# Performance work log

Hardware: AMD Instinct MI355X
Metric: run time of the kernel (lower is better)

The kernel has to match this reference:

```python
import jax, jax.numpy as jnp
import numpy as np

B, S, D, H = 8, 1024, 768, 12
DH = D // H


def setup_inputs() -> dict:
    key = jax.random.key(0)
    ks = jax.random.split(key, 6)
    scale = 1.0 / np.sqrt(D)
    return {
        "inputs": jax.random.normal(ks[0], (B, S, D), dtype=jnp.float32),
        "Wq": jax.random.normal(ks[1], (D, D), dtype=jnp.float32) * scale,
        "bq": jnp.zeros((D,), jnp.float32),
        "Wk": jax.random.normal(ks[2], (D, D), dtype=jnp.float32) * scale,
        "bk": jnp.zeros((D,), jnp.float32),
        "Wv": jax.random.normal(ks[3], (D, D), dtype=jnp.float32) * scale,
        "bv": jnp.zeros((D,), jnp.float32),
        "Wo": jax.random.normal(ks[4], (D, D), dtype=jnp.float32) * scale,
        "bo": jnp.zeros((D,), jnp.float32),
    }


def _split_heads(x):
    # [B,S,D] -> [B,H,S,DH]
    b, s, _ = x.shape
    return x.reshape(b, s, H, DH).transpose(0, 2, 1, 3)


def reference(inputs, Wq, bq, Wk, bk, Wv, bv, Wo, bo):
    q = _split_heads(inputs @ Wq + bq)
    k = _split_heads(inputs @ Wk + bk)
    v = _split_heads(inputs @ Wv + bv)
    # scaled dot-product attention; scale = sqrt(projection_dim)
    scores = jnp.einsum("bhqd,bhkd->bhqk", q, k) / jnp.sqrt(jnp.float32(DH))
    weights = jax.nn.softmax(scores, axis=-1)
    attn = jnp.einsum("bhqk,bhkd->bhqd", weights, v)
    attn = attn.transpose(0, 2, 1, 3).reshape(inputs.shape[0], -1, D)
    return attn @ Wo + bo
```

## Files before the change

kernel.cpp:

```cpp
#include <hip/hip_runtime.h>
#include <math.h>

#define B 8
#define S 1024
#define D 768
#define H 12
#define DH 64
#define M_TOT (B * S)

typedef short bf16x8 __attribute__((ext_vector_type(8)));
typedef float f32x4 __attribute__((ext_vector_type(4)));

__device__ __forceinline__ unsigned short f2bf(float x) {
    unsigned u = __builtin_bit_cast(unsigned, x);
    u = (u + 0x7FFFu + ((u >> 16) & 1u)) >> 16;
    return (unsigned short)u;
}
__device__ __forceinline__ unsigned pk2bf(float a, float b) {
    return (unsigned)f2bf(a) | ((unsigned)f2bf(b) << 16);
}

__device__ __forceinline__ void async16(const unsigned short* g, unsigned short* l) {
    __builtin_amdgcn_global_load_lds((const __attribute__((address_space(1))) void*)g,
                                     (__attribute__((address_space(3))) void*)l, 16, 0, 0);
}

__global__ __launch_bounds__(256) void conv_bf16(const float* __restrict__ src,
                                                 unsigned short* __restrict__ dst) {
    const int i = (blockIdx.x * 256 + threadIdx.x) * 4;
    const float4 v = *(const float4*)&src[i];
    ushort4 o;
    o.x = f2bf(v.x); o.y = f2bf(v.y); o.z = f2bf(v.z); o.w = f2bf(v.w);
    *(ushort4*)&dst[i] = o;
}

__global__ __launch_bounds__(256) void wtrans(const float* W0, const float* W1,
                                              const float* W2, const float* W3,
                                              unsigned short* T0, unsigned short* T1,
                                              unsigned short* T2, unsigned short* T3) {
    const float* Wsrc[4] = {W0, W1, W2, W3};
    unsigned short* Tdst[4] = {T0, T1, T2, T3};
    const float* Wm = Wsrc[blockIdx.z];
    unsigned short* Tm = Tdst[blockIdx.z];
    __shared__ float tile[64][65];
    const int t = threadIdx.x;
    const int r = t >> 4, c4 = (t & 15) * 4;
    const int k0 = blockIdx.x * 64, n0 = blockIdx.y * 64;
#pragma unroll
    for (int rr = 0; rr < 4; ++rr) {
        const float4 v = *(const float4*)&Wm[(size_t)(k0 + r + rr * 16) * D + n0 + c4];
        tile[r + rr * 16][c4 + 0] = v.x;
        tile[r + rr * 16][c4 + 1] = v.y;
        tile[r + rr * 16][c4 + 2] = v.z;
        tile[r + rr * 16][c4 + 3] = v.w;
    }
    __syncthreads();
#pragma unroll
    for (int rr = 0; rr < 4; ++rr) {
        const int nr = r + rr * 16;
        ushort4 o;
        o.x = f2bf(tile[c4 + 0][nr]);
        o.y = f2bf(tile[c4 + 1][nr]);
        o.z = f2bf(tile[c4 + 2][nr]);
        o.w = f2bf(tile[c4 + 3][nr]);
        *(ushort4*)&Tm[(size_t)(n0 + nr) * D + k0 + c4] = o;
    }
}

__global__ __launch_bounds__(256) void gemm_qkv(const unsigned short* __restrict__ A,
                                                const unsigned short* __restrict__ Wtq,
                                                const unsigned short* __restrict__ Wtk,
                                                const unsigned short* __restrict__ Wtv,
                                                const float* __restrict__ bq,
                                                const float* __restrict__ bk,
                                                const float* __restrict__ bv,
                                                unsigned short* __restrict__ Qb,
                                                unsigned short* __restrict__ Kb,
                                                unsigned short* __restrict__ Vtb) {
    __shared__ unsigned short At[128 * 32];
    __shared__ unsigned short Bs[128 * 32];
    const int z = blockIdx.z;
    const unsigned short* Bt = (z == 0) ? Wtq : (z == 1) ? Wtk : Wtv;
    const float* bias = (z == 0) ? bq : (z == 1) ? bk : bv;
    const float scale = (z == 0) ? 0.125f : 1.0f;

    const int t = threadIdx.x;
    const int w = t >> 6, lane = t & 63;
    const int quad = lane >> 4, l15 = lane & 15;
    const int m0 = blockIdx.x * 128, n0 = blockIdx.y * 128;
    const int wm = (w & 1) * 64, wn = (w >> 1) * 64;
    const int srow = lane >> 2, scol = (lane & 3) * 8;

    f32x4 acc[4][4];
#pragma unroll
    for (int i = 0; i < 4; ++i)
#pragma unroll
        for (int j = 0; j < 4; ++j) acc[i][j] = (f32x4){0.f, 0.f, 0.f, 0.f};

    for (int kt = 0; kt < D / 32; ++kt) {
        const int k0 = kt * 32;
        __syncthreads();
#pragma unroll
        for (int c = 0; c < 2; ++c) {
            const int cc = w * 2 + c;
            const int row = cc * 16 + srow;
            async16(&A[(size_t)(m0 + row) * D + k0 + scol], &At[cc * 512]);
            async16(&Bt[(size_t)(n0 + row) * D + k0 + scol], &Bs[cc * 512]);
        }
        __syncthreads();
        bf16x8 af[4], bfr[4];
#pragma unroll
        for (int i = 0; i < 4; ++i)
            af[i] = *(const bf16x8*)&At[(wm + i * 16 + l15) * 32 + quad * 8];
#pragma unroll
        for (int j = 0; j < 4; ++j)
            bfr[j] = *(const bf16x8*)&Bs[(wn + j * 16 + l15) * 32 + quad * 8];
#pragma unroll
        for (int i = 0; i < 4; ++i)
#pragma unroll
            for (int j = 0; j < 4; ++j)
                acc[i][j] = __builtin_amdgcn_mfma_f32_16x16x32_bf16(af[i], bfr[j], acc[i][j], 0, 0, 0);
    }

#pragma unroll
    for (int j = 0; j < 4; ++j) {
        const int col = n0 + wn + j * 16 + l15;
        const float bv2 = bias[col];
#pragma unroll
        for (int i = 0; i < 4; ++i) {
            const int row0 = m0 + wm + i * 16 + quad * 4;
            if (z < 2) {
                unsigned short* C = (z == 0) ? Qb : Kb;
#pragma unroll
                for (int r = 0; r < 4; ++r)
                    C[(size_t)(row0 + r) * D + col] = f2bf((acc[i][j][r] + bv2) * scale);
            } else {
                const int h = col >> 6, dh = col & 63;
                const int bb = row0 >> 10, s0 = row0 & 1023;
                ushort4 o;
                o.x = f2bf(acc[i][j][0] + bv2);
                o.y = f2bf(acc[i][j][1] + bv2);
                o.z = f2bf(acc[i][j][2] + bv2);
                o.w = f2bf(acc[i][j][3] + bv2);
                *(ushort4*)&Vtb[((size_t)(bb * H + h) * DH + dh) * S + s0] = o;
            }
        }
    }
}

__global__ __launch_bounds__(256) void gemm_out(const unsigned short* __restrict__ A,
                                                const unsigned short* __restrict__ Bt,
                                                const float* __restrict__ bias,
                                                float* __restrict__ C) {
    __shared__ unsigned short At[128 * 32];
    __shared__ unsigned short Bs[128 * 32];
    const int t = threadIdx.x;
    const int w = t >> 6, lane = t & 63;
    const int quad = lane >> 4, l15 = lane & 15;
    const int m0 = blockIdx.x * 128, n0 = blockIdx.y * 128;
    const int wm = (w & 1) * 64, wn = (w >> 1) * 64;
    const int srow = lane >> 2, scol = (lane & 3) * 8;

    f32x4 acc[4][4];
#pragma unroll
    for (int i = 0; i < 4; ++i)
#pragma unroll
        for (int j = 0; j < 4; ++j) acc[i][j] = (f32x4){0.f, 0.f, 0.f, 0.f};

    for (int kt = 0; kt < D / 32; ++kt) {
        const int k0 = kt * 32;
        __syncthreads();
#pragma unroll
        for (int c = 0; c < 2; ++c) {
            const int cc = w * 2 + c;
            const int row = cc * 16 + srow;
            async16(&A[(size_t)(m0 + row) * D + k0 + scol], &At[cc * 512]);
            async16(&Bt[(size_t)(n0 + row) * D + k0 + scol], &Bs[cc * 512]);
        }
        __syncthreads();
        bf16x8 af[4], bfr[4];
#pragma unroll
        for (int i = 0; i < 4; ++i)
            af[i] = *(const bf16x8*)&At[(wm + i * 16 + l15) * 32 + quad * 8];
#pragma unroll
        for (int j = 0; j < 4; ++j)
            bfr[j] = *(const bf16x8*)&Bs[(wn + j * 16 + l15) * 32 + quad * 8];
#pragma unroll
        for (int i = 0; i < 4; ++i)
#pragma unroll
            for (int j = 0; j < 4; ++j)
                acc[i][j] = __builtin_amdgcn_mfma_f32_16x16x32_bf16(af[i], bfr[j], acc[i][j], 0, 0, 0);
    }

#pragma unroll
    for (int j = 0; j < 4; ++j) {
        const int col = n0 + wn + j * 16 + l15;
        const float bv = bias[col];
#pragma unroll
        for (int i = 0; i < 4; ++i) {
            const int row0 = m0 + wm + i * 16 + quad * 4;
#pragma unroll
            for (int r = 0; r < 4; ++r) C[(size_t)(row0 + r) * D + col] = acc[i][j][r] + bv;
        }
    }
}

__global__ __launch_bounds__(256) void attn_mfma(const unsigned short* __restrict__ Qg,
                                                 const unsigned short* __restrict__ Kg,
                                                 const unsigned short* __restrict__ Vtg,
                                                 unsigned short* __restrict__ ATT) {
    __shared__ unsigned short Ks[2 * 64 * 32];
    __shared__ unsigned short Vs[2 * 64 * 32];
    __shared__ unsigned short Ps2[4 * 32 * 72];

    const int t = threadIdx.x;
    const int w = t >> 6, lane = t & 63;
    const int quad = lane >> 4, l15 = lane & 15;
    const int bh = blockIdx.x % (B * H);
    const int q0 = (blockIdx.x / (B * H)) * 128;
    const int b = bh / H, h = bh % H;

    bf16x8 qb[2][2];
#pragma unroll
    for (int qh = 0; qh < 2; ++qh) {
        const size_t qoff = ((size_t)(b * S + q0 + w * 32 + qh * 16 + l15)) * D + h * DH;
        qb[qh][0] = *(const bf16x8*)&Qg[qoff + quad * 8];
        qb[qh][1] = *(const bf16x8*)&Qg[qoff + 32 + quad * 8];
    }

    f32x4 o[2][4];
#pragma unroll
    for (int qh = 0; qh < 2; ++qh)
#pragma unroll
        for (int n = 0; n < 4; ++n) o[qh][n] = (f32x4){0.f, 0.f, 0.f, 0.f};
    float m_r[2] = {-INFINITY, -INFINITY};
    float l_r[2] = {0.f, 0.f};

    const int srow = lane >> 2;
    const int scol = (((lane & 3) ^ ((lane >> 3) & 3))) * 8;
    const int fsw = ((quad ^ ((l15 >> 1) & 3)) * 8);

    unsigned short* myP = &Ps2[w * 32 * 72];

    for (int kt = 0; kt < S / 64; ++kt) {
        __syncthreads();
#pragma unroll
        for (int kc = 0; kc < 2; ++kc) {
            async16(&Kg[((size_t)(b * S + kt * 64 + w * 16 + srow)) * D + h * DH + kc * 32 + scol],
                    &Ks[kc * 2048 + w * 512]);
            async16(&Vtg[((size_t)(bh * DH + w * 16 + srow)) * S + kt * 64 + kc * 32 + scol],
                    &Vs[kc * 2048 + w * 512]);
        }
        __syncthreads();

        f32x4 sc[2][4];
#pragma unroll
        for (int n = 0; n < 4; ++n) {
            const bf16x8 ka0 = *(const bf16x8*)&Ks[0 * 2048 + (n * 16 + l15) * 32 + fsw];
            const bf16x8 ka1 = *(const bf16x8*)&Ks[1 * 2048 + (n * 16 + l15) * 32 + fsw];
#pragma unroll
            for (int qh = 0; qh < 2; ++qh) {
                f32x4 zz = (f32x4){0.f, 0.f, 0.f, 0.f};
                zz = __builtin_amdgcn_mfma_f32_16x16x32_bf16(ka0, qb[qh][0], zz, 0, 0, 0);
                zz = __builtin_amdgcn_mfma_f32_16x16x32_bf16(ka1, qb[qh][1], zz, 0, 0, 0);
                sc[qh][n] = zz;
            }
        }

        float alpha[2];
#pragma unroll
        for (int qh = 0; qh < 2; ++qh) {
            float rmax = -INFINITY;
#pragma unroll
            for (int n = 0; n < 4; ++n)
#pragma unroll
                for (int r = 0; r < 4; ++r) rmax = fmaxf(rmax, sc[qh][n][r]);
            rmax = fmaxf(rmax, __shfl_xor(rmax, 16, 64));
            rmax = fmaxf(rmax, __shfl_xor(rmax, 32, 64));
            const float mnew = fmaxf(m_r[qh], rmax);
            alpha[qh] = __expf(m_r[qh] - mnew);
            m_r[qh] = mnew;
            float rsum = 0.f;
#pragma unroll
            for (int n = 0; n < 4; ++n) {
                uint2 u;
                float p0 = __expf(sc[qh][n][0] - mnew);
                float p1 = __expf(sc[qh][n][1] - mnew);
                float p2 = __expf(sc[qh][n][2] - mnew);
                float p3 = __expf(sc[qh][n][3] - mnew);
                rsum += (p0 + p1) + (p2 + p3);
                u.x = pk2bf(p0, p1);
                u.y = pk2bf(p2, p3);
                *(uint2*)&myP[(qh * 16 + l15) * 72 + n * 16 + quad * 4] = u;
            }
            rsum += __shfl_xor(rsum, 16, 64);
            rsum += __shfl_xor(rsum, 32, 64);
            l_r[qh] = l_r[qh] * alpha[qh] + rsum;
#pragma unroll
            for (int n = 0; n < 4; ++n) o[qh][n] *= alpha[qh];
        }
        __asm__ volatile("s_waitcnt lgkmcnt(0)" ::: "memory");

        bf16x8 pb[2][2];
#pragma unroll
        for (int qh = 0; qh < 2; ++qh) {
            pb[qh][0] = *(const bf16x8*)&myP[(qh * 16 + l15) * 72 + 0 + quad * 8];
            pb[qh][1] = *(const bf16x8*)&myP[(qh * 16 + l15) * 72 + 32 + quad * 8];
        }

#pragma unroll
        for (int n = 0; n < 4; ++n) {
            const bf16x8 va0 = *(const bf16x8*)&Vs[0 * 2048 + (n * 16 + l15) * 32 + fsw];
            const bf16x8 va1 = *(const bf16x8*)&Vs[1 * 2048 + (n * 16 + l15) * 32 + fsw];
#pragma unroll
            for (int qh = 0; qh < 2; ++qh) {
                o[qh][n] = __builtin_amdgcn_mfma_f32_16x16x32_bf16(va0, pb[qh][0], o[qh][n], 0, 0, 0);
                o[qh][n] = __builtin_amdgcn_mfma_f32_16x16x32_bf16(va1, pb[qh][1], o[qh][n], 0, 0, 0);
            }
        }
    }

#pragma unroll
    for (int qh = 0; qh < 2; ++qh) {
        const float inv = 1.0f / l_r[qh];
        const size_t row = (size_t)(b * S + q0 + w * 32 + qh * 16 + l15) * D + h * DH;
#pragma unroll
        for (int n = 0; n < 4; ++n) {
            ushort4 ov;
            ov.x = f2bf(o[qh][n][0] * inv);
            ov.y = f2bf(o[qh][n][1] * inv);
            ov.z = f2bf(o[qh][n][2] * inv);
            ov.w = f2bf(o[qh][n][3] * inv);
            *(ushort4*)&ATT[row + n * 16 + quad * 4] = ov;
        }
    }
}

extern "C" void kernel_launch(void* const* d_in, const int* in_sizes, int n_in,
                              void* d_out, int out_size, void* d_ws, size_t ws_size,
                              hipStream_t stream) {
    const float* inputs = (const float*)d_in[0];
    const float* Wq = (const float*)d_in[1];
    const float* bq = (const float*)d_in[2];
    const float* Wk = (const float*)d_in[3];
    const float* bk = (const float*)d_in[4];
    const float* Wv = (const float*)d_in[5];
    const float* bv = (const float*)d_in[6];
    const float* Wo = (const float*)d_in[7];
    const float* bo = (const float*)d_in[8];

    const size_t nA = (size_t)M_TOT * D;
    unsigned short* Abf  = (unsigned short*)d_ws;
    unsigned short* Qb   = Abf + nA;
    unsigned short* Kb   = Qb + nA;
    unsigned short* Vtb  = Kb + nA;
    unsigned short* ATTb = Vtb + nA;
    unsigned short* Wtq  = ATTb + nA;
    unsigned short* Wtk  = Wtq + (size_t)D * D;
    unsigned short* Wtv  = Wtk + (size_t)D * D;
    unsigned short* Wto  = Wtv + (size_t)D * D;

    conv_bf16<<<M_TOT * D / 1024, 256, 0, stream>>>(inputs, Abf);
    wtrans<<<dim3(D / 64, D / 64, 4), 256, 0, stream>>>(Wq, Wk, Wv, Wo, Wtq, Wtk, Wtv, Wto);

    gemm_qkv<<<dim3(M_TOT / 128, D / 128, 3), 256, 0, stream>>>(
        Abf, Wtq, Wtk, Wtv, bq, bk, bv, Qb, Kb, Vtb);

    attn_mfma<<<dim3((S / 128) * B * H), 256, 0, stream>>>(Qb, Kb, Vtb, ATTb);

    gemm_out<<<dim3(M_TOT / 128, D / 128), 256, 0, stream>>>(ATTb, Wto, bo, (float*)d_out);
}
```

Before: 231.6 us.

## Double-buffer GEMM LDS tiles with async prefetch and merge prep kernels

Both projection GEMMs now use two LDS buffers: the next K-tile is loaded with global_load_lds while MFMAs run on the current one, and a partial vmcnt wait replaces the full sync. This hides global load latency that was previously exposed between two barriers. The bf16 input conversion and weight transpose kernels are also merged into one launch to save a kernel launch. The LDS footprint doubles and correctness depends on the hand-written vmcnt/s_barrier ordering.

```diff
diff --git a/kernel.cpp b/kernel.cpp
--- a/kernel.cpp
+++ b/kernel.cpp
@@ -25,45 +25,64 @@
                                      (__attribute__((address_space(3))) void*)l, 16, 0, 0);
 }
 
-__global__ __launch_bounds__(256) void conv_bf16(const float* __restrict__ src,
-                                                 unsigned short* __restrict__ dst) {
-    const int i = (blockIdx.x * 256 + threadIdx.x) * 4;
-    const float4 v = *(const float4*)&src[i];
-    ushort4 o;
-    o.x = f2bf(v.x); o.y = f2bf(v.y); o.z = f2bf(v.z); o.w = f2bf(v.w);
-    *(ushort4*)&dst[i] = o;
-}
-
-__global__ __launch_bounds__(256) void wtrans(const float* W0, const float* W1,
-                                              const float* W2, const float* W3,
-                                              unsigned short* T0, unsigned short* T1,
-                                              unsigned short* T2, unsigned short* T3) {
-    const float* Wsrc[4] = {W0, W1, W2, W3};
-    unsigned short* Tdst[4] = {T0, T1, T2, T3};
-    const float* Wm = Wsrc[blockIdx.z];
-    unsigned short* Tm = Tdst[blockIdx.z];
-    __shared__ float tile[64][65];
+__device__ __forceinline__ void stage_tiles(const unsigned short* __restrict__ A,
+                                            const unsigned short* __restrict__ Bt,
+                                            unsigned short* At, unsigned short* Bs,
+                                            int m0, int n0, int k0, int w, int srow, int scol) {
+#pragma unroll
+    for (int c = 0; c < 2; ++c) {
+        const int cc = w * 2 + c;
+        const int row = cc * 16 + srow;
+        async16(&A[(size_t)(m0 + row) * D + k0 + scol], &At[cc * 512]);
+        async16(&Bt[(size_t)(n0 + row) * D + k0 + scol], &Bs[cc * 512]);
+    }
+}
+
+__global__ __launch_bounds__(256) void prep(const float* __restrict__ inputs,
+                                            unsigned short* __restrict__ Abf,
+                                            const float* W0, const float* W1,
+                                            const float* W2, const float* W3,
+                                            unsigned short* T0, unsigned short* T1,
+                                            unsigned short* T2, unsigned short* T3) {
+    const int bid = blockIdx.x;
     const int t = threadIdx.x;
-    const int r = t >> 4, c4 = (t & 15) * 4;
-    const int k0 = blockIdx.x * 64, n0 = blockIdx.y * 64;
-#pragma unroll
-    for (int rr = 0; rr < 4; ++rr) {
-        const float4 v = *(const float4*)&Wm[(size_t)(k0 + r + rr * 16) * D + n0 + c4];
-        tile[r + rr * 16][c4 + 0] = v.x;
-        tile[r + rr * 16][c4 + 1] = v.y;
-        tile[r + rr * 16][c4 + 2] = v.z;
-        tile[r + rr * 16][c4 + 3] = v.w;
-    }
-    __syncthreads();
-#pragma unroll
-    for (int rr = 0; rr < 4; ++rr) {
-        const int nr = r + rr * 16;
+    if (bid < 6144) {
+        const int i = (bid * 256 + t) * 4;
+        const float4 v = *(const float4*)&inputs[i];
         ushort4 o;
-        o.x = f2bf(tile[c4 + 0][nr]);
-        o.y = f2bf(tile[c4 + 1][nr]);
-        o.z = f2bf(tile[c4 + 2][nr]);
-        o.w = f2bf(tile[c4 + 3][nr]);
-        *(ushort4*)&Tm[(size_t)(n0 + nr) * D + k0 + c4] = o;
+        o.x = f2bf(v.x); o.y = f2bf(v.y); o.z = f2bf(v.z); o.w = f2bf(v.w);
+        *(ushort4*)&Abf[i] = o;
+    } else {
+        const int id = bid - 6144;
+        const int z = id / 144;
+        const int rem = id % 144;
+        const int kx = rem % 12, ny = rem / 12;
+        const float* Wsrc[4] = {W0, W1, W2, W3};
+        unsigned short* Tdst[4] = {T0, T1, T2, T3};
+        const float* Wm = Wsrc[z];
+        unsigned short* Tm = Tdst[z];
+        __shared__ float tile[64][65];
+        const int r = t >> 4, c4 = (t & 15) * 4;
+        const int k0 = kx * 64, n0 = ny * 64;
+#pragma unroll
+        for (int rr = 0; rr < 4; ++rr) {
+            const float4 v = *(const float4*)&Wm[(size_t)(k0 + r + rr * 16) * D + n0 + c4];
+            tile[r + rr * 16][c4 + 0] = v.x;
+            tile[r + rr * 16][c4 + 1] = v.y;
+            tile[r + rr * 16][c4 + 2] = v.z;
+            tile[r + rr * 16][c4 + 3] = v.w;
+        }
+        __syncthreads();
+#pragma unroll
+        for (int rr = 0; rr < 4; ++rr) {
+            const int nr = r + rr * 16;
+            ushort4 o;
+            o.x = f2bf(tile[c4 + 0][nr]);
+            o.y = f2bf(tile[c4 + 1][nr]);
+            o.z = f2bf(tile[c4 + 2][nr]);
+            o.w = f2bf(tile[c4 + 3][nr]);
+            *(ushort4*)&Tm[(size_t)(n0 + nr) * D + k0 + c4] = o;
+        }
     }
 }
 
@@ -77,8 +96,8 @@
                                                 unsigned short* __restrict__ Qb,
                                                 unsigned short* __restrict__ Kb,
                                                 unsigned short* __restrict__ Vtb) {
-    __shared__ unsigned short At[128 * 32];
-    __shared__ unsigned short Bs[128 * 32];
+    __shared__ unsigned short At[2][128 * 32];
+    __shared__ unsigned short Bs[2][128 * 32];
     const int z = blockIdx.z;
     const unsigned short* Bt = (z == 0) ? Wtq : (z == 1) ? Wtk : Wtv;
     const float* bias = (z == 0) ? bq : (z == 1) ? bk : bv;
@@ -97,29 +116,30 @@
 #pragma unroll
         for (int j = 0; j < 4; ++j) acc[i][j] = (f32x4){0.f, 0.f, 0.f, 0.f};
 
+    stage_tiles(A, Bt, At[0], Bs[0], m0, n0, 0, w, srow, scol);
     for (int kt = 0; kt < D / 32; ++kt) {
-        const int k0 = kt * 32;
-        __syncthreads();
-#pragma unroll
-        for (int c = 0; c < 2; ++c) {
-            const int cc = w * 2 + c;
-            const int row = cc * 16 + srow;
-            async16(&A[(size_t)(m0 + row) * D + k0 + scol], &At[cc * 512]);
-            async16(&Bt[(size_t)(n0 + row) * D + k0 + scol], &Bs[cc * 512]);
-        }
-        __syncthreads();
+        unsigned short* Atc = At[kt & 1];
+        unsigned short* Bsc = Bs[kt & 1];
+        if (kt + 1 < D / 32) {
+            stage_tiles(A, Bt, At[(kt + 1) & 1], Bs[(kt + 1) & 1], m0, n0, (kt + 1) * 32, w, srow, scol);
+            __asm__ volatile("s_waitcnt vmcnt(4)" ::: "memory");
+        } else {
+            __asm__ volatile("s_waitcnt vmcnt(0)" ::: "memory");
+        }
+        __asm__ volatile("s_barrier" ::: "memory");
         bf16x8 af[4], bfr[4];
 #pragma unroll
         for (int i = 0; i < 4; ++i)
-            af[i] = *(const bf16x8*)&At[(wm + i * 16 + l15) * 32 + quad * 8];
+            af[i] = *(const bf16x8*)&Atc[(wm + i * 16 + l15) * 32 + quad * 8];
 #pragma unroll
         for (int j = 0; j < 4; ++j)
-            bfr[j] = *(const bf16x8*)&Bs[(wn + j * 16 + l15) * 32 + quad * 8];
+            bfr[j] = *(const bf16x8*)&Bsc[(wn + j * 16 + l15) * 32 + quad * 8];
 #pragma unroll
         for (int i = 0; i < 4; ++i)
 #pragma unroll
             for (int j = 0; j < 4; ++j)
                 acc[i][j] = __builtin_amdgcn_mfma_f32_16x16x32_bf16(af[i], bfr[j], acc[i][j], 0, 0, 0);
+        __asm__ volatile("s_barrier" ::: "memory");
     }
 
 #pragma unroll
@@ -152,8 +172,8 @@
                                                 const unsigned short* __restrict__ Bt,
                                                 const float* __restrict__ bias,
                                                 float* __restrict__ C) {
-    __shared__ unsigned short At[128 * 32];
-    __shared__ unsigned short Bs[128 * 32];
+    __shared__ unsigned short At[2][128 * 32];
+    __shared__ unsigned short Bs[2][128 * 32];
     const int t = threadIdx.x;
     const int w = t >> 6, lane = t & 63;
     const int quad = lane >> 4, l15 = lane & 15;
@@ -167,29 +187,30 @@
 #pragma unroll
         for (int j = 0; j < 4; ++j) acc[i][j] = (f32x4){0.f, 0.f, 0.f, 0.f};
 
+    stage_tiles(A, Bt, At[0], Bs[0], m0, n0, 0, w, srow, scol);
     for (int kt = 0; kt < D / 32; ++kt) {
-        const int k0 = kt * 32;
-        __syncthreads();
-#pragma unroll
-        for (int c = 0; c < 2; ++c) {
-            const int cc = w * 2 + c;
-            const int row = cc * 16 + srow;
-            async16(&A[(size_t)(m0 + row) * D + k0 + scol], &At[cc * 512]);
-            async16(&Bt[(size_t)(n0 + row) * D + k0 + scol], &Bs[cc * 512]);
-        }
-        __syncthreads();
+        unsigned short* Atc = At[kt & 1];
+        unsigned short* Bsc = Bs[kt & 1];
+        if (kt + 1 < D / 32) {
+            stage_tiles(A, Bt, At[(kt + 1) & 1], Bs[(kt + 1) & 1], m0, n0, (kt + 1) * 32, w, srow, scol);
+            __asm__ volatile("s_waitcnt vmcnt(4)" ::: "memory");
+        } else {
+            __asm__ volatile("s_waitcnt vmcnt(0)" ::: "memory");
+        }
+        __asm__ volatile("s_barrier" ::: "memory");
         bf16x8 af[4], bfr[4];
 #pragma unroll
         for (int i = 0; i < 4; ++i)
-            af[i] = *(const bf16x8*)&At[(wm + i * 16 + l15) * 32 + quad * 8];
+            af[i] = *(const bf16x8*)&Atc[(wm + i * 16 + l15) * 32 + quad * 8];
 #pragma unroll
         for (int j = 0; j < 4; ++j)
-            bfr[j] = *(const bf16x8*)&Bs[(wn + j * 16 + l15) * 32 + quad * 8];
+            bfr[j] = *(const bf16x8*)&Bsc[(wn + j * 16 + l15) * 32 + quad * 8];
 #pragma unroll
         for (int i = 0; i < 4; ++i)
 #pragma unroll
             for (int j = 0; j < 4; ++j)
                 acc[i][j] = __builtin_amdgcn_mfma_f32_16x16x32_bf16(af[i], bfr[j], acc[i][j], 0, 0, 0);
+        __asm__ volatile("s_barrier" ::: "memory");
     }
 
 #pragma unroll
@@ -360,8 +381,7 @@
     unsigned short* Wtv  = Wtk + (size_t)D * D;
     unsigned short* Wto  = Wtv + (size_t)D * D;
 
-    conv_bf16<<<M_TOT * D / 1024, 256, 0, stream>>>(inputs, Abf);
-    wtrans<<<dim3(D / 64, D / 64, 4), 256, 0, stream>>>(Wq, Wk, Wv, Wo, Wtq, Wtk, Wtv, Wto);
+    prep<<<6144 + 576, 256, 0, stream>>>(inputs, Abf, Wq, Wk, Wv, Wo, Wtq, Wtk, Wtv, Wto);
 
     gemm_qkv<<<dim3(M_TOT / 128, D / 128, 3), 256, 0, stream>>>(
         Abf, Wtq, Wtk, Wtv, bq, bk, bv, Qb, Kb, Vtb);
```

New measurement: 222.4 us. 4.0% less time.
